# Kernel tuning notes

Measured on AMD Instinct MI355X. Metric: run time of the kernel, lower is better.

Reference implementation:

```python
import jax, jax.numpy as jnp
import numpy as np

EPS = 1e-12  # torch F.normalize default eps
N_SLOTS, KEY_DIM, HID = 128, 40, 200


def setup_inputs() -> dict:
    key = jax.random.key(0)
    ks = jax.random.split(key, 12)
    T, D, F = 4096, 512, 256
    s = lambda fan: 1.0 / np.sqrt(fan)
    return {
        "x_train": jax.random.normal(ks[0], (T, D), jnp.float32),
        "y_train": jax.random.normal(ks[1], (T, 1), jnp.float32),
        "W_in": jax.random.normal(ks[2], (D, F), jnp.float32) * s(D),
        "b_in": jnp.zeros((F,), jnp.float32),
        "W_ih": jax.random.normal(ks[3], (4 * HID, F + 1), jnp.float32) * s(HID),
        "W_hh": jax.random.normal(ks[4], (4 * HID, HID), jnp.float32) * s(HID),
        "b_ih": jnp.zeros((4 * HID,), jnp.float32),
        "b_hh": jnp.zeros((4 * HID,), jnp.float32),
        "W_k": jax.random.normal(ks[5], (HID, KEY_DIM), jnp.float32) * s(HID),
        "b_k": jnp.zeros((KEY_DIM,), jnp.float32),
        "W_s": jax.random.normal(ks[6], (HID, 1), jnp.float32) * s(HID),
        "b_s": jnp.zeros((1,), jnp.float32),
        "gamma": jnp.full((1,), 0.95, jnp.float32),
    }


def _forward(x_train, y_train, W_in, b_in, W_ih, W_hh, b_ih, b_hh, W_k, b_k, W_s, b_s, gamma):
    dt = x_train.dtype
    xs = x_train @ W_in + b_in                                   # [T, F]
    # y shifted by one step (pad a zero row at front, drop last)
    y_shift = jnp.concatenate([jnp.zeros((1, 1), dt), y_train[:-1]], axis=0)
    xys = jnp.concatenate([xs, y_shift], axis=1)                 # [T, F+1]

    def lstm_step(carry, x):
        h, c = carry
        g = x @ W_ih.T + h @ W_hh.T + b_ih + b_hh                # [4H]
        i, f, gg, o = jnp.split(g, 4)
        c = jax.nn.sigmoid(f) * c + jax.nn.sigmoid(i) * jnp.tanh(gg)
        h = jax.nn.sigmoid(o) * jnp.tanh(c)
        return (h, c), h

    h0 = (jnp.zeros((HID,), dt), jnp.zeros((HID,), dt))
    _, hiddens = jax.lax.scan(lstm_step, h0, xys)                # [T, H]

    keys = jnp.tanh(hiddens @ W_k + b_k)                         # [T, K]
    sigmas = jax.nn.sigmoid(hiddens @ W_s + b_s)[:, 0]           # [T]

    M0 = 1e-6 * jnp.ones((N_SLOTS, KEY_DIM), dt)
    w0 = jnp.zeros((N_SLOTS,), dt).at[0].set(1.0)
    g = gamma[0]

    def mann_step(carry, inp):
        M, wr, wu = carry
        k, sigma = inp
        wlu = (wu <= jnp.max(wu)).astype(dt)                     # least-used mask
        ww = sigma * wr + (1.0 - sigma) * wlu                    # write weights
        M = M + ww[:, None] * k[None, :]                         # outer-product write
        Mn = M / jnp.maximum(jnp.linalg.norm(M, axis=1, keepdims=True), EPS)
        # torch normalize(k.unsqueeze(1)) normalizes dim=1 of [K,1] -> elementwise sign
        kn = k / jnp.maximum(jnp.abs(k), EPS)
        wr = jax.nn.softmax(Mn @ kn)                             # [N]
        wu = g * wu + wr + ww
        return (M, wr, wu), None

    (M_T, wr_T, wu_T), _ = jax.lax.scan(mann_step, (M0, w0, w0), (keys, sigmas))
    return M_T


def reference(x_train, y_train, W_in, b_in, W_ih, W_hh, b_ih, b_hh, W_k, b_k, W_s, b_s, gamma):
    return _forward(x_train, y_train, W_in, b_in, W_ih, W_hh, b_ih, b_hh, W_k, b_k, W_s, b_s, gamma)
```

## Files before the change

### kernel.cpp

```cpp
#include <hip/hip_runtime.h>
#include <hip/hip_bf16.h>

#define T_STEPS 4096
#define D_IN    512
#define F_DIM   256
#define HID     200
#define G4      800
#define KDIM    40
#define NSLOT   128

#define TPW    7
#define KT     7
#define CH     16
#define NCHUNK 256
#define NWORK  62

typedef _Float16 f16x8 __attribute__((ext_vector_type(8)));
typedef float    f32x4 __attribute__((ext_vector_type(4)));

__device__ __forceinline__ float ldin(const void* p, long i, int bf) {
  if (bf) {
    unsigned v = ((unsigned)((const unsigned short*)p)[i]) << 16;
    return __uint_as_float(v);
  }
  return ((const float*)p)[i];
}

__device__ __forceinline__ unsigned short f2bf(float x) {
  unsigned b = __float_as_uint(x);
  b = (b + 0x7FFFu + ((b >> 16) & 1u)) >> 16;
  return (unsigned short)b;
}

__device__ __forceinline__ float frcp(float x) { return __builtin_amdgcn_rcpf(x); }
__device__ __forceinline__ float frsq(float x) { return __builtin_amdgcn_rsqf(x); }

__device__ __forceinline__ float dppq_xor1(float x) {
  return __int_as_float(__builtin_amdgcn_update_dpp(
      0, __float_as_int(x), 0xB1, 0xF, 0xF, false));
}
__device__ __forceinline__ float dppq_xor2(float x) {
  return __int_as_float(__builtin_amdgcn_update_dpp(
      0, __float_as_int(x), 0x4E, 0xF, 0xF, false));
}

__device__ __forceinline__ void gload_lds16(const float* g, float* lds) {
  __builtin_amdgcn_global_load_lds(
      (const __attribute__((address_space(1))) unsigned int*)g,
      (__attribute__((address_space(3))) unsigned int*)lds, 16, 0, 0);
}

__device__ __forceinline__ int kmap(int grp, int e) {
  return (e < 4) ? (4 * grp + e) : (16 + 4 * grp + (e - 4));
}

__device__ __forceinline__ float wave_sum64(float v) {
  v += __int_as_float(__builtin_amdgcn_update_dpp(0, __float_as_int(v), 0x121, 0xF, 0xF, 0));
  v += __int_as_float(__builtin_amdgcn_update_dpp(0, __float_as_int(v), 0x122, 0xF, 0xF, 0));
  v += __int_as_float(__builtin_amdgcn_update_dpp(0, __float_as_int(v), 0x124, 0xF, 0xF, 0));
  v += __int_as_float(__builtin_amdgcn_update_dpp(0, __float_as_int(v), 0x128, 0xF, 0xF, 0));
  v += __int_as_float(__builtin_amdgcn_ds_swizzle(__float_as_int(v), 0x401F));
  v += __shfl_xor(v, 32, 64);
  return v;
}

__device__ __forceinline__ void spin_flag(const unsigned* f) {
  if (__hip_atomic_load(f, __ATOMIC_RELAXED, __HIP_MEMORY_SCOPE_AGENT) == 0u) {
    while (__hip_atomic_load(f, __ATOMIC_RELAXED, __HIP_MEMORY_SCOPE_AGENT) == 0u)
      __builtin_amdgcn_s_sleep(2);
  }
  (void)__hip_atomic_load(f, __ATOMIC_ACQUIRE, __HIP_MEMORY_SCOPE_AGENT);
}
__device__ __forceinline__ void set_flag(unsigned* f) {
  __hip_atomic_store(f, 1u, __ATOMIC_RELEASE, __HIP_MEMORY_SCOPE_AGENT);
}

__global__ void detect_mode_k(const void* gamma, int* flag) {
  unsigned u32 = ((const unsigned*)gamma)[0];
  float asf  = __uint_as_float(u32);
  float asbf = __uint_as_float(((unsigned)((const unsigned short*)gamma)[0]) << 16);
  int m = 0;
  if (asf > 0.90f && asf < 1.0f) m = 0;
  else if (asbf > 0.90f && asbf < 1.0f) m = 1;
  *flag = m;
}

__global__ __launch_bounds__(256) void xs_k(const void* x, const void* Win, const void* bin,
                                            float* xs, const int* flagp) {
  int bf = *flagp;
  int f = threadIdx.x;
  int t0 = blockIdx.x * 8;
  __shared__ float xl[8][D_IN];
  for (int idx = threadIdx.x; idx < 8 * D_IN; idx += 256)
    xl[idx >> 9][idx & 511] = ldin(x, (long)(t0 + (idx >> 9)) * D_IN + (idx & 511), bf);
  __syncthreads();
  float acc[8];
  float bv = ldin(bin, f, bf);
#pragma unroll
  for (int i = 0; i < 8; ++i) acc[i] = bv;
  for (int k = 0; k < D_IN; ++k) {
    float w = ldin(Win, (long)k * F_DIM + f, bf);
#pragma unroll
    for (int i = 0; i < 8; ++i) acc[i] += xl[i][k] * w;
  }
#pragma unroll
  for (int i = 0; i < 8; ++i) xs[(long)(t0 + i) * F_DIM + f] = acc[i];
}

struct SmemLstm {
  float gbuf[2][CH][G4];
  float hh[2][CH][HID];
  _Float16 h_fr[2][224];
};
struct SmemWork {
  float xl[CH][F_DIM];
  float yl[CH];
};
struct SmemCons {
  float WkT[KDIM][HID];
  float Wsl[HID];
  float hl[CH][HID];
  float rc[CH][96];
};
union SmemU { SmemLstm l; SmemWork w; SmemCons c; };

__global__ __launch_bounds__(512, 2) void fused_k(
    const void* Whh, const void* Wih, const void* bih, const void* bhh,
    const void* y, const float* xs,
    const void* Wk, const void* bk, const void* Ws, const void* bs,
    float* gpre, float* hid, void* out,
    unsigned* fg, unsigned* fh, const int* flagp) {
  __shared__ SmemU sm;
  int bf = *flagp;
  int bid = blockIdx.x;
  int tid = threadIdx.x;

  if (bid >= 2) {
    for (int c = bid - 2; c < NCHUNK; c += NWORK) {
      int t0 = c * CH;
      for (int i = tid; i < CH * F_DIM / 4; i += 512)
        ((float4*)sm.w.xl)[i] = ((const float4*)(xs + (long)t0 * F_DIM))[i];
      if (tid < CH) {
        int t = t0 + tid;
        sm.w.yl[tid] = (t == 0) ? 0.f : ldin(y, t - 1, bf);
      }
      __syncthreads();
      for (int j = tid; j < G4; j += 512) {
        int gate = j / 200, unit = j - gate * 200;
        int jv = 4 * unit + gate;
        float base = ldin(bih, j, bf) + ldin(bhh, j, bf);
        float acc[CH];
#pragma unroll
        for (int s = 0; s < CH; ++s) acc[s] = base;
        for (int f4 = 0; f4 < F_DIM / 4; ++f4) {
          float w0 = ldin(Wih, (long)j * 257 + 4 * f4 + 0, bf);
          float w1 = ldin(Wih, (long)j * 257 + 4 * f4 + 1, bf);
          float w2 = ldin(Wih, (long)j * 257 + 4 * f4 + 2, bf);
          float w3 = ldin(Wih, (long)j * 257 + 4 * f4 + 3, bf);
#pragma unroll
          for (int s = 0; s < CH; ++s) {
            float4 xv = *((const float4*)sm.w.xl[s] + f4);
            acc[s] = fmaf(xv.x, w0, acc[s]);
            acc[s] = fmaf(xv.y, w1, acc[s]);
            acc[s] = fmaf(xv.z, w2, acc[s]);
            acc[s] = fmaf(xv.w, w3, acc[s]);
          }
        }
        float wy = ldin(Wih, (long)j * 257 + 256, bf);
#pragma unroll
        for (int s = 0; s < CH; ++s)
          gpre[(long)(t0 + s) * G4 + jv] = fmaf(sm.w.yl[s], wy, acc[s]);
      }
      __syncthreads();
      if (tid == 0) set_flag(&fg[c]);
    }
    return;
  }

  if (bid == 1) {
    for (int i = tid; i < KDIM * HID; i += 512) {
      int kk = i / HID, u = i - kk * HID;
      ((float*)sm.c.WkT)[i] = ldin(Wk, (long)u * KDIM + kk, bf);
    }
    for (int i = tid; i < HID; i += 512) sm.c.Wsl[i] = ldin(Ws, i, bf);
    __syncthreads();

    float M0[KDIM], M1[KDIM];
#pragma unroll
    for (int q = 0; q < KDIM; ++q) { M0[q] = 1e-6f; M1[q] = 1e-6f; }
    float nsq0 = 4.0e-11f, nsq1 = 4.0e-11f;
    float wr0 = (tid == 0) ? 1.f : 0.f, wr1 = 0.f;

    for (int c = 0; c < NCHUNK; ++c) {
      spin_flag(&fh[c]);
      for (int i = tid; i < CH * HID / 4; i += 512)
        ((float4*)sm.c.hl)[i] = ((const float4*)(hid + (long)c * CH * HID))[i];
      __syncthreads();

      for (int task = tid; task < CH * 41; task += 512) {
        int s = task / 41, kk = task - s * 41;
        const float4* hp = (const float4*)sm.c.hl[s];
        if (kk < KDIM) {
          float acc = ldin(bk, kk, bf);
          const float4* wp = (const float4*)sm.c.WkT[kk];
#pragma unroll
          for (int u4 = 0; u4 < HID / 4; ++u4) {
            float4 hv = hp[u4], wv = wp[u4];
            acc = fmaf(hv.x, wv.x, acc);
            acc = fmaf(hv.y, wv.y, acc);
            acc = fmaf(hv.z, wv.z, acc);
            acc = fmaf(hv.w, wv.w, acc);
          }
          float kv = tanhf(acc);
          float kn = kv / fmaxf(fabsf(kv), 1e-12f);
          sm.c.rc[s][kk] = kv;
          sm.c.rc[s][KDIM + kk] = kn;
        } else {
          float acc = ldin(bs, 0, bf);
          const float4* wp = (const float4*)sm.c.Wsl;
#pragma unroll
          for (int u4 = 0; u4 < HID / 4; ++u4) {
            float4 hv = hp[u4], wv = wp[u4];
            acc = fmaf(hv.x, wv.x, acc);
            acc = fmaf(hv.y, wv.y, acc);
            acc = fmaf(hv.z, wv.z, acc);
            acc = fmaf(hv.w, wv.w, acc);
          }
          sm.c.rc[s][80] = 1.f / (1.f + expf(-acc));
        }
      }
      __syncthreads();
      if (tid < CH) {
        const float4* rp = (const float4*)sm.c.rc[tid];
        float c2 = 0.f, c3 = 0.f;
#pragma unroll
        for (int q = 0; q < 10; ++q) {
          float4 kv = rp[q], kn = rp[10 + q];
          c2 = fmaf(kv.x, kn.x, c2); c2 = fmaf(kv.y, kn.y, c2);
          c2 = fmaf(kv.z, kn.z, c2); c2 = fmaf(kv.w, kn.w, c2);
          c3 = fmaf(kv.x, kv.x, c3); c3 = fmaf(kv.y, kv.y, c3);
          c3 = fmaf(kv.z, kv.z, c3); c3 = fmaf(kv.w, kv.w, c3);
        }
        sm.c.rc[tid][81] = c2;
        sm.c.rc[tid][82] = c3;
        sm.c.rc[tid][83] = 0.f;
      }
      __syncthreads();

      if (tid < 64) {
        for (int s = 0; s < CH; ++s) {
          const float4* rp = (const float4*)sm.c.rc[s];
          float4 ex = rp[20];
          float sg = ex.x;
          float ww0 = fmaf(sg, wr0, 1.f - sg);
          float ww1 = fmaf(sg, wr1, 1.f - sg);
          float4 a0 = {0,0,0,0}, b0 = {0,0,0,0}, a1 = {0,0,0,0}, b1 = {0,0,0,0};
#pragma unroll
          for (int q = 0; q < 10; ++q) {
            float4 kv = rp[q], kn = rp[10 + q];
            float m00 = M0[4*q+0], m01 = M0[4*q+1], m02 = M0[4*q+2], m03 = M0[4*q+3];
            float m10 = M1[4*q+0], m11 = M1[4*q+1], m12 = M1[4*q+2], m13 = M1[4*q+3];
            a0.x = fmaf(m00, kn.x, a0.x); a0.y = fmaf(m01, kn.y, a0.y);
            a0.z = fmaf(m02, kn.z, a0.z); a0.w = fmaf(m03, kn.w, a0.w);
            b0.x = fmaf(m00, kv.x, b0.x); b0.y = fmaf(m01, kv.y, b0.y);
            b0.z = fmaf(m02, kv.z, b0.z); b0.w = fmaf(m03, kv.w, b0.w);
            a1.x = fmaf(m10, kn.x, a1.x); a1.y = fmaf(m11, kn.y, a1.y);
            a1.z = fmaf(m12, kn.z, a1.z); a1.w = fmaf(m13, kn.w, a1.w);
            b1.x = fmaf(m10, kv.x, b1.x); b1.y = fmaf(m11, kv.y, b1.y);
            b1.z = fmaf(m12, kv.z, b1.z); b1.w = fmaf(m13, kv.w, b1.w);
            M0[4*q+0] = fmaf(ww0, kv.x, m00); M0[4*q+1] = fmaf(ww0, kv.y, m01);
            M0[4*q+2] = fmaf(ww0, kv.z, m02); M0[4*q+3] = fmaf(ww0, kv.w, m03);
            M1[4*q+0] = fmaf(ww1, kv.x, m10); M1[4*q+1] = fmaf(ww1, kv.y, m11);
            M1[4*q+2] = fmaf(ww1, kv.z, m12); M1[4*q+3] = fmaf(ww1, kv.w, m13);
          }
          float D10 = (a0.x + a0.y) + (a0.z + a0.w);
          float D20 = (b0.x + b0.y) + (b0.z + b0.w);
          float D11 = (a1.x + a1.y) + (a1.z + a1.w);
          float D21 = (b1.x + b1.y) + (b1.z + b1.w);
          if ((s & 7) == 7) {
            float4 r0 = {0,0,0,0}, r1 = {0,0,0,0};
#pragma unroll
            for (int q = 0; q < 10; ++q) {
              r0.x = fmaf(M0[4*q+0], M0[4*q+0], r0.x);
              r0.y = fmaf(M0[4*q+1], M0[4*q+1], r0.y);
              r0.z = fmaf(M0[4*q+2], M0[4*q+2], r0.z);
              r0.w = fmaf(M0[4*q+3], M0[4*q+3], r0.w);
              r1.x = fmaf(M1[4*q+0], M1[4*q+0], r1.x);
              r1.y = fmaf(M1[4*q+1], M1[4*q+1], r1.y);
              r1.z = fmaf(M1[4*q+2], M1[4*q+2], r1.z);
              r1.w = fmaf(M1[4*q+3], M1[4*q+3], r1.w);
            }
            nsq0 = (r0.x + r0.y) + (r0.z + r0.w);
            nsq1 = (r1.x + r1.y) + (r1.z + r1.w);
          } else {
            nsq0 = fmaf(ww0 * ww0, ex.z, fmaf(2.f * ww0, D20, nsq0));
            nsq1 = fmaf(ww1 * ww1, ex.z, fmaf(2.f * ww1, D21, nsq1));
          }
          float dot0 = fmaf(ww0, ex.y, D10);
          float dot1 = fmaf(ww1, ex.y, D11);
          float v0 = dot0 * frsq(fmaxf(nsq0, 1e-24f));
          float v1 = dot1 * frsq(fmaxf(nsq1, 1e-24f));
          float e0 = __expf(v0), e1 = __expf(v1);
          float es = wave_sum64(e0 + e1);
          float ri = frcp(es);
          wr0 = e0 * ri;
          wr1 = e1 * ri;
        }
      }
    }
    if (tid < 64) {
#pragma unroll
      for (int q = 0; q < KDIM; ++q) {
        long i0 = (long)tid * KDIM + q;
        long i1 = (long)(tid + 64) * KDIM + q;
        if (bf) {
          ((unsigned short*)out)[i0] = f2bf(M0[q]);
          ((unsigned short*)out)[i1] = f2bf(M1[q]);
        } else {
          ((float*)out)[i0] = M0[q];
          ((float*)out)[i1] = M1[q];
        }
      }
    }
    return;
  }

  int lane = tid & 63, wid = tid >> 6;
  int col = lane & 15, grp = (lane >> 4) & 3;
  int g = col & 3;
  int qq = col >> 2;

  for (int i = tid; i < 448; i += 512) ((_Float16*)sm.l.h_fr)[i] = (_Float16)0.f;

  bool isg2 = (g == 2);
  float sx = isg2 ? 2.f : -1.f;
  float am = isg2 ? -2.f : 1.f;
  float ab = isg2 ? 1.f : 0.f;

  f16x8 fB[TPW][KT];
#pragma unroll
  for (int it = 0; it < TPW; ++it) {
    int t = wid + 8 * it;
    bool ok = (t < 50);
    int u = 4 * t + qq;
    long rowbase = (long)(200 * g + (ok ? u : 0)) * HID;
#pragma unroll
    for (int kt = 0; kt < KT; ++kt) {
      f16x8 v;
#pragma unroll
      for (int e = 0; e < 8; ++e) {
        int k = kt * 32 + kmap(grp, e);
        float w = (ok && k < HID) ? ldin(Whh, rowbase + k, bf) : 0.f;
        v[e] = (_Float16)w;
      }
      fB[it][kt] = v;
    }
  }

  int t0_ = wid + 8 * grp;
  int t1_ = wid + 32 + 8 * grp;
  bool val1 = (grp < 3) && (t1_ < 50);
  int u0 = 4 * t0_ + qq, u1 = val1 ? (4 * t1_ + qq) : 0;
  int vv0 = 16 * t0_ + col;
  int vv1 = val1 ? (16 * t1_ + col) : 0;
  int pos0, pos1;
  {
    int r = u0 & 31;
    pos0 = (u0 >> 5) * 32 + ((r < 16) ? ((r >> 2) * 8 + (r & 3))
                                      : (((r - 16) >> 2) * 8 + 4 + ((r - 16) & 3)));
    r = u1 & 31;
    pos1 = (u1 >> 5) * 32 + ((r < 16) ? ((r >> 2) * 8 + (r & 3))
                                      : (((r - 16) >> 2) * 8 + 4 + ((r - 16) & 3)));
  }
  bool wrt = (g == 0);
  bool w2 = (wid < 2);

  spin_flag(&fg[0]);
  {
    float* dst = (float*)sm.l.gbuf[0];
    for (int sl = wid; sl < 50; sl += 8)
      gload_lds16(gpre + sl * 256 + lane * 4, dst + sl * 256);
  }
  __syncthreads();

  float cst0 = 0.f, cst1 = 0.f;
  int p = 0;
  for (int tc = 0; tc < T_STEPS; tc += CH) {
    int pb = (tc >> 4) & 1;
    int cn = tc / CH + 1;
    if (cn < NCHUNK) {
      spin_flag(&fg[cn]);
      const float* src = gpre + (long)(tc + CH) * G4;
      float* dst = (float*)sm.l.gbuf[pb ^ 1];
      for (int sl = wid; sl < 50; sl += 8)
        gload_lds16(src + sl * 256 + lane * 4, dst + sl * 256);
    }
    for (int s = 0; s < CH; ++s) {
      f16x8 a7[KT];
#pragma unroll
      for (int kt = 0; kt < KT; ++kt)
        a7[kt] = *(const f16x8*)&sm.l.h_fr[p][kt * 32 + grp * 8];
      float gb0 = sm.l.gbuf[pb][s][vv0];
      float gb1 = sm.l.gbuf[pb][s][vv1];

      f32x4 ac0 = {0,0,0,0}, ac1 = {0,0,0,0}, ac2 = {0,0,0,0}, ac3 = {0,0,0,0};
      f32x4 ac4 = {0,0,0,0}, ac5 = {0,0,0,0}, ac6 = {0,0,0,0};
#pragma unroll
      for (int kt = 0; kt < KT; ++kt) {
        f16x8 a = a7[kt];
        ac0 = __builtin_amdgcn_mfma_f32_16x16x32_f16(a, fB[0][kt], ac0, 0, 0, 0);
        ac1 = __builtin_amdgcn_mfma_f32_16x16x32_f16(a, fB[1][kt], ac1, 0, 0, 0);
        ac2 = __builtin_amdgcn_mfma_f32_16x16x32_f16(a, fB[2][kt], ac2, 0, 0, 0);
        ac3 = __builtin_amdgcn_mfma_f32_16x16x32_f16(a, fB[3][kt], ac3, 0, 0, 0);
        ac4 = __builtin_amdgcn_mfma_f32_16x16x32_f16(a, fB[4][kt], ac4, 0, 0, 0);
        ac5 = __builtin_amdgcn_mfma_f32_16x16x32_f16(a, fB[5][kt], ac5, 0, 0, 0);
      }
      if (w2) {
#pragma unroll
        for (int kt = 0; kt < KT; ++kt)
          ac6 = __builtin_amdgcn_mfma_f32_16x16x32_f16(a7[kt], fB[6][kt], ac6, 0, 0, 0);
      }
      float pj_r0 = (grp == 0) ? ac0[0] : (grp == 1) ? ac1[0] : (grp == 2) ? ac2[0] : ac3[0];
      float pj_r1 = (grp == 0) ? ac4[0] : (grp == 1) ? ac5[0] : ac6[0];

      {
        float pre = pj_r0 + gb0;
        float yv = __expf(sx * pre);
        float z = frcp(1.f + yv);
        float act = fmaf(am, z, ab);
        float s1 = dppq_xor1(act);
        float a_e = (g & 1) ? s1 : act;
        float a_o = (g & 1) ? act : s1;
        float b_e = dppq_xor2(a_e);
        float b_o = dppq_xor2(a_o);
        float si = (g & 2) ? b_e : a_e;
        float sf = (g & 2) ? b_o : a_o;
        float tg = (g & 2) ? a_e : b_e;
        float so = (g & 2) ? a_o : b_o;
        float c = fmaf(sf, cst0, si * tg);
        cst0 = c;
        float th = 1.f - 2.f * frcp(1.f + __expf(2.f * c));
        float h = so * th;
        if (wrt) {
          sm.l.h_fr[p ^ 1][pos0] = (_Float16)h;
          sm.l.hh[pb][s][u0] = h;
        }
      }
      {
        float pre = pj_r1 + gb1;
        float yv = __expf(sx * pre);
        float z = frcp(1.f + yv);
        float act = fmaf(am, z, ab);
        float s1 = dppq_xor1(act);
        float a_e = (g & 1) ? s1 : act;
        float a_o = (g & 1) ? act : s1;
        float b_e = dppq_xor2(a_e);
        float b_o = dppq_xor2(a_o);
        float si = (g & 2) ? b_e : a_e;
        float sf = (g & 2) ? b_o : a_o;
        float tg = (g & 2) ? a_e : b_e;
        float so = (g & 2) ? a_o : b_o;
        float c = fmaf(sf, cst1, si * tg);
        cst1 = c;
        float th = 1.f - 2.f * frcp(1.f + __expf(2.f * c));
        float h = so * th;
        if (wrt && val1) {
          sm.l.h_fr[p ^ 1][pos1] = (_Float16)h;
          sm.l.hh[pb][s][u1] = h;
        }
      }
      __syncthreads();
      p ^= 1;
    }
    {
      const float4* src = (const float4*)sm.l.hh[pb];
      float4* dst = (float4*)(hid + (long)tc * HID);
      for (int i = tid; i < CH * HID / 4; i += 512) dst[i] = src[i];
    }
    __syncthreads();
    if (tid == 0) set_flag(&fh[tc / CH]);
  }
}

extern "C" void kernel_launch(void* const* d_in, const int* in_sizes, int n_in,
                              void* d_out, int out_size, void* d_ws, size_t ws_size,
                              hipStream_t stream) {
  const void* x_train = d_in[0];
  const void* y_train = d_in[1];
  const void* W_in = d_in[2];
  const void* b_in = d_in[3];
  const void* W_ih = d_in[4];
  const void* W_hh = d_in[5];
  const void* b_ih = d_in[6];
  const void* b_hh = d_in[7];
  const void* W_k  = d_in[8];
  const void* b_k  = d_in[9];
  const void* W_s  = d_in[10];
  const void* b_s  = d_in[11];
  const void* gamma = d_in[12];

  char* ws = (char*)d_ws;
  int*      flag = (int*)ws;
  unsigned* fg   = (unsigned*)(ws + 256);
  unsigned* fh   = (unsigned*)(ws + 1280);
  float*    gpre = (float*)(ws + 4096);
  float*    hid  = (float*)(ws + 4096 + 13107200L);
  float*    xs   = (float*)(ws + 4096 + 13107200L + 3276800L);

  detect_mode_k<<<1, 1, 0, stream>>>(gamma, flag);
  hipMemsetAsync(ws + 256, 0, 2048, stream);
  xs_k<<<512, 256, 0, stream>>>(x_train, W_in, b_in, xs, flag);
  fused_k<<<64, 512, 0, stream>>>(W_hh, W_ih, b_ih, b_hh, y_train, xs,
                                  W_k, b_k, W_s, b_s,
                                  gpre, hid, d_out, fg, fh, flag);
}
```

Baseline: 5.289 ms.

## Shrink LSTM recurrence block to four waves with thirteen MFMA tiles each

Cuts the fused kernel to 256 threads per block. Each of the four LSTM waves now holds 13 W_hh fragment tiles in registers and computes up to four hidden units per lane group. The goal is a cheaper per-timestep __syncthreads across fewer waves on the serial recurrence path. In exchange each wave issues twice the MFMAs per step, register pressure rises sharply, and the worker and consumer blocks lose half their threads.

```diff
diff --git a/kernel.cpp b/kernel.cpp
--- a/kernel.cpp
+++ b/kernel.cpp
@@ -9,7 +9,7 @@
 #define KDIM    40
 #define NSLOT   128
 
-#define TPW    7
+#define TPW    13
 #define KT     7
 #define CH     16
 #define NCHUNK 256
@@ -124,7 +124,7 @@
 };
 union SmemU { SmemLstm l; SmemWork w; SmemCons c; };
 
-__global__ __launch_bounds__(512, 2) void fused_k(
+__global__ __launch_bounds__(256, 1) void fused_k(
     const void* Whh, const void* Wih, const void* bih, const void* bhh,
     const void* y, const float* xs,
     const void* Wk, const void* bk, const void* Ws, const void* bs,
@@ -138,14 +138,14 @@
   if (bid >= 2) {
     for (int c = bid - 2; c < NCHUNK; c += NWORK) {
       int t0 = c * CH;
-      for (int i = tid; i < CH * F_DIM / 4; i += 512)
+      for (int i = tid; i < CH * F_DIM / 4; i += 256)
         ((float4*)sm.w.xl)[i] = ((const float4*)(xs + (long)t0 * F_DIM))[i];
       if (tid < CH) {
         int t = t0 + tid;
         sm.w.yl[tid] = (t == 0) ? 0.f : ldin(y, t - 1, bf);
       }
       __syncthreads();
-      for (int j = tid; j < G4; j += 512) {
+      for (int j = tid; j < G4; j += 256) {
         int gate = j / 200, unit = j - gate * 200;
         int jv = 4 * unit + gate;
         float base = ldin(bih, j, bf) + ldin(bhh, j, bf);
@@ -178,11 +178,11 @@
   }
 
   if (bid == 1) {
-    for (int i = tid; i < KDIM * HID; i += 512) {
+    for (int i = tid; i < KDIM * HID; i += 256) {
       int kk = i / HID, u = i - kk * HID;
       ((float*)sm.c.WkT)[i] = ldin(Wk, (long)u * KDIM + kk, bf);
     }
-    for (int i = tid; i < HID; i += 512) sm.c.Wsl[i] = ldin(Ws, i, bf);
+    for (int i = tid; i < HID; i += 256) sm.c.Wsl[i] = ldin(Ws, i, bf);
     __syncthreads();
 
     float M0[KDIM], M1[KDIM];
@@ -193,11 +193,11 @@
 
     for (int c = 0; c < NCHUNK; ++c) {
       spin_flag(&fh[c]);
-      for (int i = tid; i < CH * HID / 4; i += 512)
+      for (int i = tid; i < CH * HID / 4; i += 256)
         ((float4*)sm.c.hl)[i] = ((const float4*)(hid + (long)c * CH * HID))[i];
       __syncthreads();
 
-      for (int task = tid; task < CH * 41; task += 512) {
+      for (int task = tid; task < CH * 41; task += 256) {
         int s = task / 41, kk = task - s * 41;
         const float4* hp = (const float4*)sm.c.hl[s];
         if (kk < KDIM) {
@@ -330,7 +330,7 @@
   int g = col & 3;
   int qq = col >> 2;
 
-  for (int i = tid; i < 448; i += 512) ((_Float16*)sm.l.h_fr)[i] = (_Float16)0.f;
+  for (int i = tid; i < 448; i += 256) ((_Float16*)sm.l.h_fr)[i] = (_Float16)0.f;
 
   bool isg2 = (g == 2);
   float sx = isg2 ? 2.f : -1.f;
@@ -340,7 +340,7 @@
   f16x8 fB[TPW][KT];
 #pragma unroll
   for (int it = 0; it < TPW; ++it) {
-    int t = wid + 8 * it;
+    int t = wid + 4 * it;
     bool ok = (t < 50);
     int u = 4 * t + qq;
     long rowbase = (long)(200 * g + (ok ? u : 0)) * HID;
@@ -357,33 +357,32 @@
     }
   }
 
-  int t0_ = wid + 8 * grp;
-  int t1_ = wid + 32 + 8 * grp;
-  bool val1 = (grp < 3) && (t1_ < 50);
-  int u0 = 4 * t0_ + qq, u1 = val1 ? (4 * t1_ + qq) : 0;
-  int vv0 = 16 * t0_ + col;
-  int vv1 = val1 ? (16 * t1_ + col) : 0;
-  int pos0, pos1;
-  {
-    int r = u0 & 31;
-    pos0 = (u0 >> 5) * 32 + ((r < 16) ? ((r >> 2) * 8 + (r & 3))
-                                      : (((r - 16) >> 2) * 8 + 4 + ((r - 16) & 3)));
-    r = u1 & 31;
-    pos1 = (u1 >> 5) * 32 + ((r < 16) ? ((r >> 2) * 8 + (r & 3))
-                                      : (((r - 16) >> 2) * 8 + 4 + ((r - 16) & 3)));
+  int vv_a[4], u_a[4], pos_a[4];
+  bool val_a[4];
+#pragma unroll
+  for (int a = 0; a < 4; ++a) {
+    int it = 4 * a + grp;
+    int t = wid + 4 * it;
+    bool v_ = (it < TPW) && (t < 50);
+    val_a[a] = v_;
+    int u = v_ ? (4 * t + qq) : 0;
+    u_a[a] = u;
+    vv_a[a] = v_ ? (16 * t + col) : 0;
+    int r = u & 31;
+    pos_a[a] = (u >> 5) * 32 + ((r < 16) ? ((r >> 2) * 8 + (r & 3))
+                                         : (((r - 16) >> 2) * 8 + 4 + ((r - 16) & 3)));
   }
   bool wrt = (g == 0);
-  bool w2 = (wid < 2);
 
   spin_flag(&fg[0]);
   {
     float* dst = (float*)sm.l.gbuf[0];
-    for (int sl = wid; sl < 50; sl += 8)
+    for (int sl = wid; sl < 50; sl += 4)
       gload_lds16(gpre + sl * 256 + lane * 4, dst + sl * 256);
   }
   __syncthreads();
 
-  float cst0 = 0.f, cst1 = 0.f;
+  float cst[4] = {0.f, 0.f, 0.f, 0.f};
   int p = 0;
   for (int tc = 0; tc < T_STEPS; tc += CH) {
     int pb = (tc >> 4) & 1;
@@ -392,7 +391,7 @@
       spin_flag(&fg[cn]);
       const float* src = gpre + (long)(tc + CH) * G4;
       float* dst = (float*)sm.l.gbuf[pb ^ 1];
-      for (int sl = wid; sl < 50; sl += 8)
+      for (int sl = wid; sl < 50; sl += 4)
         gload_lds16(src + sl * 256 + lane * 4, dst + sl * 256);
     }
     for (int s = 0; s < CH; ++s) {
@@ -400,31 +399,40 @@
 #pragma unroll
       for (int kt = 0; kt < KT; ++kt)
         a7[kt] = *(const f16x8*)&sm.l.h_fr[p][kt * 32 + grp * 8];
-      float gb0 = sm.l.gbuf[pb][s][vv0];
-      float gb1 = sm.l.gbuf[pb][s][vv1];
+      float gb[4];
+#pragma unroll
+      for (int a = 0; a < 4; ++a) gb[a] = sm.l.gbuf[pb][s][vv_a[a]];
 
       f32x4 ac0 = {0,0,0,0}, ac1 = {0,0,0,0}, ac2 = {0,0,0,0}, ac3 = {0,0,0,0};
-      f32x4 ac4 = {0,0,0,0}, ac5 = {0,0,0,0}, ac6 = {0,0,0,0};
+      f32x4 ac4 = {0,0,0,0}, ac5 = {0,0,0,0}, ac6 = {0,0,0,0}, ac7 = {0,0,0,0};
+      f32x4 ac8 = {0,0,0,0}, ac9 = {0,0,0,0}, ac10 = {0,0,0,0}, ac11 = {0,0,0,0};
+      f32x4 ac12 = {0,0,0,0};
 #pragma unroll
       for (int kt = 0; kt < KT; ++kt) {
         f16x8 a = a7[kt];
-        ac0 = __builtin_amdgcn_mfma_f32_16x16x32_f16(a, fB[0][kt], ac0, 0, 0, 0);
-        ac1 = __builtin_amdgcn_mfma_f32_16x16x32_f16(a, fB[1][kt], ac1, 0, 0, 0);
-        ac2 = __builtin_amdgcn_mfma_f32_16x16x32_f16(a, fB[2][kt], ac2, 0, 0, 0);
-        ac3 = __builtin_amdgcn_mfma_f32_16x16x32_f16(a, fB[3][kt], ac3, 0, 0, 0);
-        ac4 = __builtin_amdgcn_mfma_f32_16x16x32_f16(a, fB[4][kt], ac4, 0, 0, 0);
-        ac5 = __builtin_amdgcn_mfma_f32_16x16x32_f16(a, fB[5][kt], ac5, 0, 0, 0);
-      }
-      if (w2) {
-#pragma unroll
-        for (int kt = 0; kt < KT; ++kt)
-          ac6 = __builtin_amdgcn_mfma_f32_16x16x32_f16(a7[kt], fB[6][kt], ac6, 0, 0, 0);
-      }
-      float pj_r0 = (grp == 0) ? ac0[0] : (grp == 1) ? ac1[0] : (grp == 2) ? ac2[0] : ac3[0];
-      float pj_r1 = (grp == 0) ? ac4[0] : (grp == 1) ? ac5[0] : ac6[0];
-
-      {
-        float pre = pj_r0 + gb0;
+        ac0  = __builtin_amdgcn_mfma_f32_16x16x32_f16(a, fB[0][kt],  ac0, 0, 0, 0);
+        ac1  = __builtin_amdgcn_mfma_f32_16x16x32_f16(a, fB[1][kt],  ac1, 0, 0, 0);
+        ac2  = __builtin_amdgcn_mfma_f32_16x16x32_f16(a, fB[2][kt],  ac2, 0, 0, 0);
+        ac3  = __builtin_amdgcn_mfma_f32_16x16x32_f16(a, fB[3][kt],  ac3, 0, 0, 0);
+        ac4  = __builtin_amdgcn_mfma_f32_16x16x32_f16(a, fB[4][kt],  ac4, 0, 0, 0);
+        ac5  = __builtin_amdgcn_mfma_f32_16x16x32_f16(a, fB[5][kt],  ac5, 0, 0, 0);
+        ac6  = __builtin_amdgcn_mfma_f32_16x16x32_f16(a, fB[6][kt],  ac6, 0, 0, 0);
+        ac7  = __builtin_amdgcn_mfma_f32_16x16x32_f16(a, fB[7][kt],  ac7, 0, 0, 0);
+        ac8  = __builtin_amdgcn_mfma_f32_16x16x32_f16(a, fB[8][kt],  ac8, 0, 0, 0);
+        ac9  = __builtin_amdgcn_mfma_f32_16x16x32_f16(a, fB[9][kt],  ac9, 0, 0, 0);
+        ac10 = __builtin_amdgcn_mfma_f32_16x16x32_f16(a, fB[10][kt], ac10, 0, 0, 0);
+        ac11 = __builtin_amdgcn_mfma_f32_16x16x32_f16(a, fB[11][kt], ac11, 0, 0, 0);
+        ac12 = __builtin_amdgcn_mfma_f32_16x16x32_f16(a, fB[12][kt], ac12, 0, 0, 0);
+      }
+
+#pragma unroll
+      for (int a = 0; a < 4; ++a) {
+        float pre;
+        if (a == 0) pre = (grp == 0) ? ac0[0] : (grp == 1) ? ac1[0] : (grp == 2) ? ac2[0] : ac3[0];
+        else if (a == 1) pre = (grp == 0) ? ac4[0] : (grp == 1) ? ac5[0] : (grp == 2) ? ac6[0] : ac7[0];
+        else if (a == 2) pre = (grp == 0) ? ac8[0] : (grp == 1) ? ac9[0] : (grp == 2) ? ac10[0] : ac11[0];
+        else pre = ac12[0];
+        pre += gb[a];
         float yv = __expf(sx * pre);
         float z = frcp(1.f + yv);
         float act = fmaf(am, z, ab);
@@ -437,36 +445,13 @@
         float sf = (g & 2) ? b_o : a_o;
         float tg = (g & 2) ? a_e : b_e;
         float so = (g & 2) ? a_o : b_o;
-        float c = fmaf(sf, cst0, si * tg);
-        cst0 = c;
+        float c = fmaf(sf, cst[a], si * tg);
+        cst[a] = c;
         float th = 1.f - 2.f * frcp(1.f + __expf(2.f * c));
         float h = so * th;
-        if (wrt) {
-          sm.l.h_fr[p ^ 1][pos0] = (_Float16)h;
-          sm.l.hh[pb][s][u0] = h;
-        }
-      }
-      {
-        float pre = pj_r1 + gb1;
-        float yv = __expf(sx * pre);
-        float z = frcp(1.f + yv);
-        float act = fmaf(am, z, ab);
-        float s1 = dppq_xor1(act);
-        float a_e = (g & 1) ? s1 : act;
-        float a_o = (g & 1) ? act : s1;
-        float b_e = dppq_xor2(a_e);
-        float b_o = dppq_xor2(a_o);
-        float si = (g & 2) ? b_e : a_e;
-        float sf = (g & 2) ? b_o : a_o;
-        float tg = (g & 2) ? a_e : b_e;
-        float so = (g & 2) ? a_o : b_o;
-        float c = fmaf(sf, cst1, si * tg);
-        cst1 = c;
-        float th = 1.f - 2.f * frcp(1.f + __expf(2.f * c));
-        float h = so * th;
-        if (wrt && val1) {
-          sm.l.h_fr[p ^ 1][pos1] = (_Float16)h;
-          sm.l.hh[pb][s][u1] = h;
+        if (wrt && val_a[a]) {
+          sm.l.h_fr[p ^ 1][pos_a[a]] = (_Float16)h;
+          sm.l.hh[pb][s][u_a[a]] = h;
         }
       }
       __syncthreads();
@@ -475,7 +460,7 @@
     {
       const float4* src = (const float4*)sm.l.hh[pb];
       float4* dst = (float4*)(hid + (long)tc * HID);
-      for (int i = tid; i < CH * HID / 4; i += 512) dst[i] = src[i];
+      for (int i = tid; i < CH * HID / 4; i += 256) dst[i] = src[i];
     }
     __syncthreads();
     if (tid == 0) set_flag(&fh[tc / CH]);
@@ -510,7 +495,7 @@
   detect_mode_k<<<1, 1, 0, stream>>>(gamma, flag);
   hipMemsetAsync(ws + 256, 0, 2048, stream);
   xs_k<<<512, 256, 0, stream>>>(x_train, W_in, b_in, xs, flag);
-  fused_k<<<64, 512, 0, stream>>>(W_hh, W_ih, b_ih, b_hh, y_train, xs,
+  fused_k<<<64, 256, 0, stream>>>(W_hh, W_ih, b_ih, b_hh, y_train, xs,
                                   W_k, b_k, W_s, b_s,
                                   gpre, hid, d_out, fg, fh, flag);
 }
```

Result: slower. 6.688 ms (+26.5%).
